# Kernel tuning notes

Measured on AMD Instinct MI355X. Metric: run time of the kernel, lower is better.

The kernel has to match this reference:

```python
import jax, jax.numpy as jnp
import numpy as np

B, P, L = 8, 196, 80
DIM1, DIM2, ATT = 2048, 300, 1024


def setup_inputs() -> dict:
    key = jax.random.key(0)
    ks = jax.random.split(key, 8)
    s1 = 1.0 / np.sqrt(DIM1)
    s2 = 1.0 / np.sqrt(DIM2)
    sa = 1.0 / np.sqrt(ATT)
    return {
        "x1": jax.random.normal(ks[0], (B, P, DIM1), jnp.float32),
        "x2": jax.random.normal(ks[1], (B, L, DIM2), jnp.float32),
        "W1": jax.random.uniform(ks[2], (ATT, DIM1), jnp.float32, -s1, s1),
        "W2": jax.random.uniform(ks[3], (ATT, DIM2), jnp.float32, -s2, s2),
        "Wh": jax.random.uniform(ks[4], (ATT, ATT), jnp.float32, -sa, sa),
        "bh": jax.random.uniform(ks[5], (ATT,), jnp.float32, -sa, sa),
        "wt": jax.random.uniform(ks[6], (ATT,), jnp.float32, -sa, sa),
        "bt": jax.random.uniform(ks[7], (), jnp.float32, -sa, sa),
    }


def reference(x1, x2, W1, W2, Wh, bh, wt, bt):
    # project: p1 (B,P,A), p2 (B,L,A)
    p1 = jnp.einsum("bpd,ad->bpa", x1, W1)
    p2 = jnp.einsum("bld,ad->bla", x2, W2)
    # broadcast bilinear + tanh: (B,L,P,A)
    h = jnp.tanh(p1[:, None, :, :] * p2[:, :, None, :])
    # hidden linear then target linear (rank-1 on last dim)
    t = jnp.einsum("blpa,ca->blpc", h, Wh) + bh
    alpha = jnp.einsum("blpc,c->blp", t, wt) + bt  # (B,L,P)
    return alpha
```

## Files before the change

kernel.cpp:

```cpp
#include <hip/hip_runtime.h>
#include <hip/hip_bf16.h>

static constexpr int kB   = 8;
static constexpr int kP   = 196;
static constexpr int kL   = 80;
static constexpr int kD1  = 2048;
static constexpr int kD2  = 300;
static constexpr int kD2p = 320;
static constexpr int kATT = 1024;
static constexpr int kM   = kB * kP;
static constexpr int kR2  = kB * kL;
static constexpr int kOut = kB * kL * kP;
static constexpr int kASplit = 16;
static constexpr int kAChunk = kATT / kASplit;
static constexpr int kLPer   = 5;

static constexpr float kTanhScale = 2.8853900817779268f;

__device__ __forceinline__ unsigned short f2bf(float x) {
    union { float f; unsigned int u; } c; c.f = x;
    unsigned int r = c.u + 0x7fffu + ((c.u >> 16) & 1u);
    return (unsigned short)(r >> 16);
}

typedef __attribute__((ext_vector_type(8))) short  bf16x8;
typedef __attribute__((ext_vector_type(4))) float  f32x4;

__device__ __forceinline__ void load_lds16(const void* g, void* l) {
    __builtin_amdgcn_global_load_lds(
        (const __attribute__((address_space(1))) void*)g,
        (__attribute__((address_space(3))) void*)l, 16, 0, 0);
}

static constexpr int kN4a = kM * kD1 / 4;
static constexpr int kN4b = kATT * kD1 / 4;
static constexpr int kN1  = kR2 * kD2p;
static constexpr int kN2  = kATT * kD2p;
static constexpr int kCastBlocks =
    (kN4a + kN4b + kN1 + kN2 + 255) / 256;

__global__ __launch_bounds__(256) void prep_kernel(
        const float* __restrict__ x1, unsigned short* __restrict__ x1b,
        const float* __restrict__ W1, unsigned short* __restrict__ W1b,
        const float* __restrict__ x2, unsigned short* __restrict__ x2b,
        const float* __restrict__ W2, unsigned short* __restrict__ W2b,
        const float* __restrict__ Wh, const float* __restrict__ wt,
        const float* __restrict__ bh, const float* __restrict__ bt,
        float* __restrict__ v, float* __restrict__ beta) {
    if (blockIdx.x >= kCastBlocks) {
        int bid = blockIdx.x - kCastBlocks;
        int ax  = bid & 3;
        int c0  = (bid >> 2) * 64;
        int a   = ax * 256 + threadIdx.x;
        float acc = 0.0f;
        #pragma unroll 8
        for (int c = c0; c < c0 + 64; ++c)
            acc = fmaf(wt[c], Wh[(size_t)c * kATT + a], acc);
        atomicAdd(&v[a], acc);
        if (ax == 0 && threadIdx.x < 64) {
            int c = c0 + threadIdx.x;
            float pb = wt[c] * bh[c];
            #pragma unroll
            for (int off = 32; off > 0; off >>= 1)
                pb += __shfl_down(pb, off, 64);
            if (threadIdx.x == 0) {
                if (c0 == 0) pb += bt[0];
                atomicAdd(beta, pb);
            }
        }
        return;
    }
    int i = blockIdx.x * 256 + threadIdx.x;
    if (i < kN4a) {
        float4 f = ((const float4*)x1)[i];
        ushort4 o = { f2bf(f.x), f2bf(f.y), f2bf(f.z), f2bf(f.w) };
        ((ushort4*)x1b)[i] = o;
    } else if ((i -= kN4a) < kN4b) {
        float4 f = ((const float4*)W1)[i];
        ushort4 o = { f2bf(f.x), f2bf(f.y), f2bf(f.z), f2bf(f.w) };
        ((ushort4*)W1b)[i] = o;
    } else if ((i -= kN4b) < kN1) {
        int r = i / kD2p, c = i - r * kD2p;
        x2b[i] = (c < kD2) ? f2bf(x2[(size_t)r * kD2 + c]) : (unsigned short)0;
    } else if ((i -= kN1) < kN2) {
        int r = i / kD2p, c = i - r * kD2p;
        W2b[i] = (c < kD2) ? f2bf(W2[(size_t)r * kD2 + c]) : (unsigned short)0;
    }
}

static constexpr int kP2Blocks = (kR2 / 64) * (kATT / 64);
static constexpr int kP1Blocks = ((kM + 63) / 64) * (kATT / 64);

__global__ __launch_bounds__(256) void gemm_all_kernel(
        const unsigned short* __restrict__ x2b, const unsigned short* __restrict__ W2b,
        float* __restrict__ p2w,
        const unsigned short* __restrict__ x1b, const unsigned short* __restrict__ W1b,
        float* __restrict__ p1w) {
    __shared__ unsigned short As[64 * 64];
    __shared__ unsigned short Bs[64 * 64];

    const unsigned short *Ab, *Bb;
    float* Co; int M, K, mx, nx; float scale;
    {
        int bid = blockIdx.x;
        if (bid < kP2Blocks) {
            Ab = x2b; Bb = W2b; Co = p2w; M = kR2; K = kD2p; scale = 1.0f;
            mx = bid % (kR2 / 64); nx = bid / (kR2 / 64);
        } else {
            int l = bid - kP2Blocks;
            Ab = x1b; Bb = W1b; Co = p1w; M = kM; K = kD1; scale = kTanhScale;
            mx = l % ((kM + 63) / 64); nx = l / ((kM + 63) / 64);
        }
    }
    const int m0   = mx * 64;
    const int n0   = nx * 64;
    const int tid  = threadIdx.x;
    const int lane = tid & 63;
    const int wv   = tid >> 6;
    const int mh   = (wv >> 1) * 32;
    const int nh   = (wv & 1) * 32;

    const int row0 = tid >> 3,         ko0 = (tid & 7) * 8;
    const int row1 = (tid + 256) >> 3, ko1 = (tid & 7) * 8;
    const int ar0 = min(m0 + row0, M - 1), ar1 = min(m0 + row1, M - 1);
    const int br0 = n0 + row0,             br1 = n0 + row1;

    f32x4 acc[2][2] = {};
    for (int k0 = 0; k0 < K; k0 += 64) {
        load_lds16(Ab + (size_t)ar0 * K + k0 + ko0, (char*)As + tid * 16);
        load_lds16(Ab + (size_t)ar1 * K + k0 + ko1, (char*)As + (tid + 256) * 16);
        load_lds16(Bb + (size_t)br0 * K + k0 + ko0, (char*)Bs + tid * 16);
        load_lds16(Bb + (size_t)br1 * K + k0 + ko1, (char*)Bs + (tid + 256) * 16);
        __syncthreads();

        #pragma unroll
        for (int kk = 0; kk < 2; ++kk) {
            bf16x8 af[2], bf[2];
            #pragma unroll
            for (int i = 0; i < 2; ++i) {
                int r = mh + i * 16 + (lane & 15);
                af[i] = *(const bf16x8*)((const char*)As + r * 128 + kk * 64 + (lane >> 4) * 16);
            }
            #pragma unroll
            for (int j = 0; j < 2; ++j) {
                int r = nh + j * 16 + (lane & 15);
                bf[j] = *(const bf16x8*)((const char*)Bs + r * 128 + kk * 64 + (lane >> 4) * 16);
            }
            #pragma unroll
            for (int i = 0; i < 2; ++i)
                #pragma unroll
                for (int j = 0; j < 2; ++j)
                    acc[i][j] = __builtin_amdgcn_mfma_f32_16x16x32_bf16(
                                    af[i], bf[j], acc[i][j], 0, 0, 0);
        }
        __syncthreads();
    }

    #pragma unroll
    for (int i = 0; i < 2; ++i)
        #pragma unroll
        for (int j = 0; j < 2; ++j)
            #pragma unroll
            for (int r = 0; r < 4; ++r) {
                int m = m0 + mh + i * 16 + (lane >> 4) * 4 + r;
                int n = n0 + nh + j * 16 + (lane & 15);
                if (m < M) Co[(size_t)m * kATT + n] = scale * acc[i][j][r];
            }
}

__global__ __launch_bounds__(256) void alpha_kernel(
        const float* __restrict__ p1, const float* __restrict__ p2,
        const float* __restrict__ v, float* __restrict__ part) {
    __shared__ float vs[kAChunk];
    __shared__ float sred;
    const int b     = blockIdx.y;
    const int as    = blockIdx.z;
    const int aBase = as * kAChunk;
    const int p0    = blockIdx.x * 16;
    const int tid   = threadIdx.x;
    const int tp    = tid & 15;
    const int lg    = tid >> 4;

    if (tid < kAChunk) vs[tid] = v[aBase + tid];
    __syncthreads();
    if (tid < 64) {
        float s = vs[tid & (kAChunk - 1)] * ((tid < kAChunk) ? 1.0f : 0.0f);
        s = vs[tid < kAChunk ? tid : 0];
        if (tid >= kAChunk) s = 0.0f;
        #pragma unroll
        for (int off = 32; off > 0; off >>= 1)
            s += __shfl_down(s, off, 64);
        if (tid == 0) sred = s;
    }
    __syncthreads();
    const float sumV = sred;

    const int p   = p0 + tp;
    const int gr1 = b * kP + min(p, kP - 1);
    const float* pu = p1 + (size_t)gr1 * kATT + aBase;
    const float* pw = p2 + ((size_t)(b * kL + lg * kLPer)) * kATT + aBase;

    float acc[kLPer] = {};
    #pragma unroll 2
    for (int a4 = 0; a4 < kAChunk / 4; ++a4) {
        float4 u  = *(const float4*)(pu + a4 * 4);
        float4 vv = *(const float4*)&vs[a4 * 4];
        #pragma unroll
        for (int j = 0; j < kLPer; ++j) {
            float4 w = *(const float4*)(pw + (size_t)j * kATT + a4 * 4);
            acc[j] = fmaf(vv.x, __builtin_amdgcn_rcpf(__builtin_amdgcn_exp2f(u.x * w.x) + 1.0f), acc[j]);
            acc[j] = fmaf(vv.y, __builtin_amdgcn_rcpf(__builtin_amdgcn_exp2f(u.y * w.y) + 1.0f), acc[j]);
            acc[j] = fmaf(vv.z, __builtin_amdgcn_rcpf(__builtin_amdgcn_exp2f(u.z * w.z) + 1.0f), acc[j]);
            acc[j] = fmaf(vv.w, __builtin_amdgcn_rcpf(__builtin_amdgcn_exp2f(u.w * w.w) + 1.0f), acc[j]);
        }
    }
    if (p < kP) {
        float* po = part + (size_t)as * kOut + ((size_t)b * kL + lg * kLPer) * kP + p;
        #pragma unroll
        for (int j = 0; j < kLPer; ++j)
            po[(size_t)j * kP] = sumV - 2.0f * acc[j];
    }
}

__global__ __launch_bounds__(256) void reduce_kernel(
        const float* __restrict__ part, const float* __restrict__ beta,
        float* __restrict__ out) {
    int i = blockIdx.x * 256 + threadIdx.x;
    if (i < kOut) {
        float s = beta[0];
        #pragma unroll
        for (int r = 0; r < kASplit; ++r)
            s += part[(size_t)r * kOut + i];
        out[i] = s;
    }
}

extern "C" void kernel_launch(void* const* d_in, const int* in_sizes, int n_in,
                              void* d_out, int out_size, void* d_ws, size_t ws_size,
                              hipStream_t stream) {
    const float* x1 = (const float*)d_in[0];
    const float* x2 = (const float*)d_in[1];
    const float* W1 = (const float*)d_in[2];
    const float* W2 = (const float*)d_in[3];
    const float* Wh = (const float*)d_in[4];
    const float* bh = (const float*)d_in[5];
    const float* wt = (const float*)d_in[6];
    const float* bt = (const float*)d_in[7];
    float* out = (float*)d_out;

    float* ws   = (float*)d_ws;
    float* v    = ws;
    float* beta = ws + 1024;
    float* p2w  = ws + 1088;
    float* p1w  = p2w + (size_t)kR2 * kATT;
    unsigned short* x1b = (unsigned short*)(p1w + (size_t)kM * kATT);
    unsigned short* W1b = x1b + (size_t)kM * kD1;
    unsigned short* x2b = W1b + (size_t)kATT * kD1;
    unsigned short* W2b = x2b + (size_t)kR2 * kD2p;
    float* part = (float*)(W2b + (size_t)kATT * kD2p);

    hipMemsetAsync(ws, 0, 1088 * sizeof(float), stream);

    prep_kernel<<<dim3(kCastBlocks + 64), 256, 0, stream>>>(
        x1, x1b, W1, W1b, x2, x2b, W2, W2b, Wh, wt, bh, bt, v, beta);
    gemm_all_kernel<<<dim3(kP2Blocks + kP1Blocks), 256, 0, stream>>>(
        x2b, W2b, p2w, x1b, W1b, p1w);
    alpha_kernel<<<dim3((kP + 15) / 16, kB, kASplit), 256, 0, stream>>>(
        p1w, p2w, v, part);
    reduce_kernel<<<dim3((kOut + 255) / 256), 256, 0, stream>>>(part, beta, out);
}
```

Baseline: 154.1 us.

## Fuse fp32-to-bf16 cast into GEMM tile staging and merge prep into GEMM

Drops the separate cast pass that wrote bf16 copies of x1, W1, x2 and W2 to global memory. Each GEMM block now loads fp32 tiles, converts them in registers, and writes bf16 into LDS. The v/beta reduction blocks move into the same launch, which saves one kernel launch and the bf16 round trip through memory. In exchange, staging uses plain register loads instead of direct global-to-LDS async loads, and A/B tiles are re-read and re-converted in fp32 by many blocks.

```diff
diff --git a/kernel.cpp b/kernel.cpp
--- a/kernel.cpp
+++ b/kernel.cpp
@@ -17,41 +17,119 @@
 
 static constexpr float kTanhScale = 2.8853900817779268f;
 
-__device__ __forceinline__ unsigned short f2bf(float x) {
-    union { float f; unsigned int u; } c; c.f = x;
-    unsigned int r = c.u + 0x7fffu + ((c.u >> 16) & 1u);
-    return (unsigned short)(r >> 16);
-}
-
 typedef __attribute__((ext_vector_type(8))) short  bf16x8;
 typedef __attribute__((ext_vector_type(4))) float  f32x4;
 
-__device__ __forceinline__ void load_lds16(const void* g, void* l) {
-    __builtin_amdgcn_global_load_lds(
-        (const __attribute__((address_space(1))) void*)g,
-        (__attribute__((address_space(3))) void*)l, 16, 0, 0);
-}
-
-static constexpr int kN4a = kM * kD1 / 4;
-static constexpr int kN4b = kATT * kD1 / 4;
-static constexpr int kN1  = kR2 * kD2p;
-static constexpr int kN2  = kATT * kD2p;
-static constexpr int kCastBlocks =
-    (kN4a + kN4b + kN1 + kN2 + 255) / 256;
-
-__global__ __launch_bounds__(256) void prep_kernel(
-        const float* __restrict__ x1, unsigned short* __restrict__ x1b,
-        const float* __restrict__ W1, unsigned short* __restrict__ W1b,
-        const float* __restrict__ x2, unsigned short* __restrict__ x2b,
-        const float* __restrict__ W2, unsigned short* __restrict__ W2b,
+__device__ __forceinline__ unsigned int pack_bf2(float lo, float hi) {
+    union { float f; unsigned int u; } a, b; a.f = lo; b.f = hi;
+    unsigned int rl = a.u + 0x7fffu + ((a.u >> 16) & 1u);
+    unsigned int rh = b.u + 0x7fffu + ((b.u >> 16) & 1u);
+    return (rl >> 16) | (rh & 0xffff0000u);
+}
+
+template<int KSRC, int KT>
+__device__ __forceinline__ void stage_tile(
+        const float* __restrict__ G, int row_g, int k0,
+        unsigned short* __restrict__ S, int tid) {
+    const int row = tid >> 2;
+    const int kq  = (tid & 3) * 16;
+    const float* src = G + (size_t)row_g * KSRC + k0 + kq;
+    unsigned int pk[8];
+    #pragma unroll
+    for (int j = 0; j < 4; ++j) {
+        float4 f = make_float4(0.f, 0.f, 0.f, 0.f);
+        if (KSRC == KT || k0 + kq + j * 4 + 4 <= KSRC)
+            f = *(const float4*)(src + j * 4);
+        pk[j * 2 + 0] = pack_bf2(f.x, f.y);
+        pk[j * 2 + 1] = pack_bf2(f.z, f.w);
+    }
+    uint4* dst = (uint4*)((char*)S + row * 128 + kq * 2);
+    dst[0] = make_uint4(pk[0], pk[1], pk[2], pk[3]);
+    dst[1] = make_uint4(pk[4], pk[5], pk[6], pk[7]);
+}
+
+template<int KSRC, int KT>
+__device__ __forceinline__ void gemm_body(
+        const float* __restrict__ Ag, const float* __restrict__ Bg,
+        float* __restrict__ Co, int M, float scale, int mx, int nx,
+        unsigned short* As, unsigned short* Bs) {
+    const int m0   = mx * 64;
+    const int n0   = nx * 64;
+    const int tid  = threadIdx.x;
+    const int lane = tid & 63;
+    const int wv   = tid >> 6;
+    const int mh   = (wv >> 1) * 32;
+    const int nh   = (wv & 1) * 32;
+    const int arow = min(m0 + (tid >> 2), M - 1);
+    const int brow = n0 + (tid >> 2);
+
+    f32x4 acc[2][2] = {};
+    for (int k0 = 0; k0 < KT; k0 += 64) {
+        __syncthreads();
+        stage_tile<KSRC, KT>(Ag, arow, k0, As, tid);
+        stage_tile<KSRC, KT>(Bg, brow, k0, Bs, tid);
+        __syncthreads();
+
+        #pragma unroll
+        for (int kk = 0; kk < 2; ++kk) {
+            bf16x8 af[2], bf[2];
+            #pragma unroll
+            for (int i = 0; i < 2; ++i) {
+                int r = mh + i * 16 + (lane & 15);
+                af[i] = *(const bf16x8*)((const char*)As + r * 128 + kk * 64 + (lane >> 4) * 16);
+            }
+            #pragma unroll
+            for (int j = 0; j < 2; ++j) {
+                int r = nh + j * 16 + (lane & 15);
+                bf[j] = *(const bf16x8*)((const char*)Bs + r * 128 + kk * 64 + (lane >> 4) * 16);
+            }
+            #pragma unroll
+            for (int i = 0; i < 2; ++i)
+                #pragma unroll
+                for (int j = 0; j < 2; ++j)
+                    acc[i][j] = __builtin_amdgcn_mfma_f32_16x16x32_bf16(
+                                    af[i], bf[j], acc[i][j], 0, 0, 0);
+        }
+    }
+
+    #pragma unroll
+    for (int i = 0; i < 2; ++i)
+        #pragma unroll
+        for (int j = 0; j < 2; ++j)
+            #pragma unroll
+            for (int r = 0; r < 4; ++r) {
+                int m = m0 + mh + i * 16 + (lane >> 4) * 4 + r;
+                int n = n0 + nh + j * 16 + (lane & 15);
+                if (m < M) Co[(size_t)m * kATT + n] = scale * acc[i][j][r];
+            }
+}
+
+static constexpr int kP2Blocks = (kR2 / 64) * (kATT / 64);
+static constexpr int kP1Blocks = ((kM + 63) / 64) * (kATT / 64);
+
+__global__ __launch_bounds__(256) void mega_kernel(
+        const float* __restrict__ x2, const float* __restrict__ W2,
+        float* __restrict__ p2w,
+        const float* __restrict__ x1, const float* __restrict__ W1,
+        float* __restrict__ p1w,
         const float* __restrict__ Wh, const float* __restrict__ wt,
         const float* __restrict__ bh, const float* __restrict__ bt,
         float* __restrict__ v, float* __restrict__ beta) {
-    if (blockIdx.x >= kCastBlocks) {
-        int bid = blockIdx.x - kCastBlocks;
-        int ax  = bid & 3;
-        int c0  = (bid >> 2) * 64;
-        int a   = ax * 256 + threadIdx.x;
+    __shared__ unsigned short As[64 * 64];
+    __shared__ unsigned short Bs[64 * 64];
+    const int bid = blockIdx.x;
+    if (bid < kP2Blocks) {
+        gemm_body<kD2, kD2p>(x2, W2, p2w, kR2, 1.0f,
+                             bid % (kR2 / 64), bid / (kR2 / 64), As, Bs);
+    } else if (bid < kP2Blocks + kP1Blocks) {
+        int l = bid - kP2Blocks;
+        gemm_body<kD1, kD1>(x1, W1, p1w, kM, kTanhScale,
+                            l % ((kM + 63) / 64), l / ((kM + 63) / 64), As, Bs);
+    } else {
+        int vb = bid - kP2Blocks - kP1Blocks;
+        int ax = vb & 3;
+        int c0 = (vb >> 2) * 64;
+        int a  = ax * 256 + threadIdx.x;
         float acc = 0.0f;
         #pragma unroll 8
         for (int c = c0; c < c0 + 64; ++c)
@@ -68,104 +146,7 @@
                 atomicAdd(beta, pb);
             }
         }
-        return;
-    }
-    int i = blockIdx.x * 256 + threadIdx.x;
-    if (i < kN4a) {
-        float4 f = ((const float4*)x1)[i];
-        ushort4 o = { f2bf(f.x), f2bf(f.y), f2bf(f.z), f2bf(f.w) };
-        ((ushort4*)x1b)[i] = o;
-    } else if ((i -= kN4a) < kN4b) {
-        float4 f = ((const float4*)W1)[i];
-        ushort4 o = { f2bf(f.x), f2bf(f.y), f2bf(f.z), f2bf(f.w) };
-        ((ushort4*)W1b)[i] = o;
-    } else if ((i -= kN4b) < kN1) {
-        int r = i / kD2p, c = i - r * kD2p;
-        x2b[i] = (c < kD2) ? f2bf(x2[(size_t)r * kD2 + c]) : (unsigned short)0;
-    } else if ((i -= kN1) < kN2) {
-        int r = i / kD2p, c = i - r * kD2p;
-        W2b[i] = (c < kD2) ? f2bf(W2[(size_t)r * kD2 + c]) : (unsigned short)0;
-    }
-}
-
-static constexpr int kP2Blocks = (kR2 / 64) * (kATT / 64);
-static constexpr int kP1Blocks = ((kM + 63) / 64) * (kATT / 64);
-
-__global__ __launch_bounds__(256) void gemm_all_kernel(
-        const unsigned short* __restrict__ x2b, const unsigned short* __restrict__ W2b,
-        float* __restrict__ p2w,
-        const unsigned short* __restrict__ x1b, const unsigned short* __restrict__ W1b,
-        float* __restrict__ p1w) {
-    __shared__ unsigned short As[64 * 64];
-    __shared__ unsigned short Bs[64 * 64];
-
-    const unsigned short *Ab, *Bb;
-    float* Co; int M, K, mx, nx; float scale;
-    {
-        int bid = blockIdx.x;
-        if (bid < kP2Blocks) {
-            Ab = x2b; Bb = W2b; Co = p2w; M = kR2; K = kD2p; scale = 1.0f;
-            mx = bid % (kR2 / 64); nx = bid / (kR2 / 64);
-        } else {
-            int l = bid - kP2Blocks;
-            Ab = x1b; Bb = W1b; Co = p1w; M = kM; K = kD1; scale = kTanhScale;
-            mx = l % ((kM + 63) / 64); nx = l / ((kM + 63) / 64);
-        }
-    }
-    const int m0   = mx * 64;
-    const int n0   = nx * 64;
-    const int tid  = threadIdx.x;
-    const int lane = tid & 63;
-    const int wv   = tid >> 6;
-    const int mh   = (wv >> 1) * 32;
-    const int nh   = (wv & 1) * 32;
-
-    const int row0 = tid >> 3,         ko0 = (tid & 7) * 8;
-    const int row1 = (tid + 256) >> 3, ko1 = (tid & 7) * 8;
-    const int ar0 = min(m0 + row0, M - 1), ar1 = min(m0 + row1, M - 1);
-    const int br0 = n0 + row0,             br1 = n0 + row1;
-
-    f32x4 acc[2][2] = {};
-    for (int k0 = 0; k0 < K; k0 += 64) {
-        load_lds16(Ab + (size_t)ar0 * K + k0 + ko0, (char*)As + tid * 16);
-        load_lds16(Ab + (size_t)ar1 * K + k0 + ko1, (char*)As + (tid + 256) * 16);
-        load_lds16(Bb + (size_t)br0 * K + k0 + ko0, (char*)Bs + tid * 16);
-        load_lds16(Bb + (size_t)br1 * K + k0 + ko1, (char*)Bs + (tid + 256) * 16);
-        __syncthreads();
-
-        #pragma unroll
-        for (int kk = 0; kk < 2; ++kk) {
-            bf16x8 af[2], bf[2];
-            #pragma unroll
-            for (int i = 0; i < 2; ++i) {
-                int r = mh + i * 16 + (lane & 15);
-                af[i] = *(const bf16x8*)((const char*)As + r * 128 + kk * 64 + (lane >> 4) * 16);
-            }
-            #pragma unroll
-            for (int j = 0; j < 2; ++j) {
-                int r = nh + j * 16 + (lane & 15);
-                bf[j] = *(const bf16x8*)((const char*)Bs + r * 128 + kk * 64 + (lane >> 4) * 16);
-            }
-            #pragma unroll
-            for (int i = 0; i < 2; ++i)
-                #pragma unroll
-                for (int j = 0; j < 2; ++j)
-                    acc[i][j] = __builtin_amdgcn_mfma_f32_16x16x32_bf16(
-                                    af[i], bf[j], acc[i][j], 0, 0, 0);
-        }
-        __syncthreads();
-    }
-
-    #pragma unroll
-    for (int i = 0; i < 2; ++i)
-        #pragma unroll
-        for (int j = 0; j < 2; ++j)
-            #pragma unroll
-            for (int r = 0; r < 4; ++r) {
-                int m = m0 + mh + i * 16 + (lane >> 4) * 4 + r;
-                int n = n0 + nh + j * 16 + (lane & 15);
-                if (m < M) Co[(size_t)m * kATT + n] = scale * acc[i][j][r];
-            }
+    }
 }
 
 __global__ __launch_bounds__(256) void alpha_kernel(
@@ -184,9 +165,7 @@
     if (tid < kAChunk) vs[tid] = v[aBase + tid];
     __syncthreads();
     if (tid < 64) {
-        float s = vs[tid & (kAChunk - 1)] * ((tid < kAChunk) ? 1.0f : 0.0f);
-        s = vs[tid < kAChunk ? tid : 0];
-        if (tid >= kAChunk) s = 0.0f;
+        float s = vs[tid];
         #pragma unroll
         for (int off = 32; off > 0; off >>= 1)
             s += __shfl_down(s, off, 64);
@@ -253,18 +232,12 @@
     float* beta = ws + 1024;
     float* p2w  = ws + 1088;
     float* p1w  = p2w + (size_t)kR2 * kATT;
-    unsigned short* x1b = (unsigned short*)(p1w + (size_t)kM * kATT);
-    unsigned short* W1b = x1b + (size_t)kM * kD1;
-    unsigned short* x2b = W1b + (size_t)kATT * kD1;
-    unsigned short* W2b = x2b + (size_t)kR2 * kD2p;
-    float* part = (float*)(W2b + (size_t)kATT * kD2p);
+    float* part = p1w + (size_t)kM * kATT;
 
     hipMemsetAsync(ws, 0, 1088 * sizeof(float), stream);
 
-    prep_kernel<<<dim3(kCastBlocks + 64), 256, 0, stream>>>(
-        x1, x1b, W1, W1b, x2, x2b, W2, W2b, Wh, wt, bh, bt, v, beta);
-    gemm_all_kernel<<<dim3(kP2Blocks + kP1Blocks), 256, 0, stream>>>(
-        x2b, W2b, p2w, x1b, W1b, p1w);
+    mega_kernel<<<dim3(kP2Blocks + kP1Blocks + 64), 256, 0, stream>>>(
+        x2, W2, p2w, x1, W1, p1w, Wh, wt, bh, bt, v, beta);
     alpha_kernel<<<dim3((kP + 15) / 16, kB, kASplit), 256, 0, stream>>>(
         p1w, p2w, v, part);
     reduce_kernel<<<dim3((kOut + 255) / 256), 256, 0, stream>>>(part, beta, out);
```

Measured after the change: 159.2 us. 1.03x slower.

## Fuse prep, GEMM, alpha and reduce into one cooperative persistent kernel

Applied to the files above, without the earlier changes.

Merges the four separate kernels into a single cooperative kernel with 1024 resident blocks. The stages are separated by grid-wide syncs, and the alpha tiles run in a grid-stride loop. The v and beta reductions are rewritten as block-local reductions without atomics, which removes the workspace memset. This is meant to cut launch overhead and the gaps between kernels. In exchange it adds grid.sync costs, concentrates the v computation in only 16 blocks, and keeps the four-kernel path as a fallback if the cooperative launch fails.

```diff
diff --git a/kernel.cpp b/kernel.cpp
--- a/kernel.cpp
+++ b/kernel.cpp
@@ -1,5 +1,8 @@
 #include <hip/hip_runtime.h>
 #include <hip/hip_bf16.h>
+#include <hip/hip_cooperative_groups.h>
+
+namespace cg = cooperative_groups;
 
 static constexpr int kB   = 8;
 static constexpr int kP   = 196;
@@ -14,8 +17,24 @@
 static constexpr int kASplit = 16;
 static constexpr int kAChunk = kATT / kASplit;
 static constexpr int kLPer   = 5;
+static constexpr int kAlphaTiles = 13 * kB * kASplit;
+static constexpr int kGrid = 1024;
 
 static constexpr float kTanhScale = 2.8853900817779268f;
+
+static constexpr int kP2Blocks = (kR2 / 64) * (kATT / 64);
+static constexpr int kP1Blocks = ((kM + 63) / 64) * (kATT / 64);
+static constexpr int kGemmBlocks = kP2Blocks + kP1Blocks;
+
+static constexpr int kD0i = kM * kD1 / 4;
+static constexpr int kD1i = kATT * kD1 / 4;
+static constexpr int kD2i = kR2 * kD2p;
+static constexpr int kD3i = kATT * kD2p;
+static constexpr int kCastTotal = kD0i + kD1i + kD2i + kD3i;
+static constexpr int kCastBlk0  = 17;
+
+typedef __attribute__((ext_vector_type(8))) short  bf16x8;
+typedef __attribute__((ext_vector_type(4))) float  f32x4;
 
 __device__ __forceinline__ unsigned short f2bf(float x) {
     union { float f; unsigned int u; } c; c.f = x;
@@ -23,116 +42,91 @@
     return (unsigned short)(r >> 16);
 }
 
-typedef __attribute__((ext_vector_type(8))) short  bf16x8;
-typedef __attribute__((ext_vector_type(4))) float  f32x4;
-
 __device__ __forceinline__ void load_lds16(const void* g, void* l) {
     __builtin_amdgcn_global_load_lds(
         (const __attribute__((address_space(1))) void*)g,
         (__attribute__((address_space(3))) void*)l, 16, 0, 0);
 }
 
-static constexpr int kN4a = kM * kD1 / 4;
-static constexpr int kN4b = kATT * kD1 / 4;
-static constexpr int kN1  = kR2 * kD2p;
-static constexpr int kN2  = kATT * kD2p;
-static constexpr int kCastBlocks =
-    (kN4a + kN4b + kN1 + kN2 + 255) / 256;
-
-__global__ __launch_bounds__(256) void prep_kernel(
+__device__ __forceinline__ void cast_items(int bid, int tid,
         const float* __restrict__ x1, unsigned short* __restrict__ x1b,
         const float* __restrict__ W1, unsigned short* __restrict__ W1b,
         const float* __restrict__ x2, unsigned short* __restrict__ x2b,
         const float* __restrict__ W2, unsigned short* __restrict__ W2b,
+        int nCastBlocks) {
+    for (int i = bid * 256 + tid; i < kCastTotal; i += nCastBlocks * 256) {
+        int j = i;
+        if (j < kD0i) {
+            float4 f = ((const float4*)x1)[j];
+            ushort4 o = { f2bf(f.x), f2bf(f.y), f2bf(f.z), f2bf(f.w) };
+            ((ushort4*)x1b)[j] = o;
+        } else if ((j -= kD0i) < kD1i) {
+            float4 f = ((const float4*)W1)[j];
+            ushort4 o = { f2bf(f.x), f2bf(f.y), f2bf(f.z), f2bf(f.w) };
+            ((ushort4*)W1b)[j] = o;
+        } else if ((j -= kD1i) < kD2i) {
+            int r = j / kD2p, c = j - r * kD2p;
+            x2b[j] = (c < kD2) ? f2bf(x2[(size_t)r * kD2 + c]) : (unsigned short)0;
+        } else {
+            j -= kD2i;
+            int r = j / kD2p, c = j - r * kD2p;
+            W2b[j] = (c < kD2) ? f2bf(W2[(size_t)r * kD2 + c]) : (unsigned short)0;
+        }
+    }
+}
+
+__device__ __forceinline__ void v_block(int bid, int tid,
         const float* __restrict__ Wh, const float* __restrict__ wt,
-        const float* __restrict__ bh, const float* __restrict__ bt,
-        float* __restrict__ v, float* __restrict__ beta) {
-    if (blockIdx.x >= kCastBlocks) {
-        int bid = blockIdx.x - kCastBlocks;
-        int ax  = bid & 3;
-        int c0  = (bid >> 2) * 64;
-        int a   = ax * 256 + threadIdx.x;
-        float acc = 0.0f;
-        #pragma unroll 8
-        for (int c = c0; c < c0 + 64; ++c)
-            acc = fmaf(wt[c], Wh[(size_t)c * kATT + a], acc);
-        atomicAdd(&v[a], acc);
-        if (ax == 0 && threadIdx.x < 64) {
-            int c = c0 + threadIdx.x;
-            float pb = wt[c] * bh[c];
-            #pragma unroll
-            for (int off = 32; off > 0; off >>= 1)
-                pb += __shfl_down(pb, off, 64);
-            if (threadIdx.x == 0) {
-                if (c0 == 0) pb += bt[0];
-                atomicAdd(beta, pb);
-            }
-        }
-        return;
-    }
-    int i = blockIdx.x * 256 + threadIdx.x;
-    if (i < kN4a) {
-        float4 f = ((const float4*)x1)[i];
-        ushort4 o = { f2bf(f.x), f2bf(f.y), f2bf(f.z), f2bf(f.w) };
-        ((ushort4*)x1b)[i] = o;
-    } else if ((i -= kN4a) < kN4b) {
-        float4 f = ((const float4*)W1)[i];
-        ushort4 o = { f2bf(f.x), f2bf(f.y), f2bf(f.z), f2bf(f.w) };
-        ((ushort4*)W1b)[i] = o;
-    } else if ((i -= kN4b) < kN1) {
-        int r = i / kD2p, c = i - r * kD2p;
-        x2b[i] = (c < kD2) ? f2bf(x2[(size_t)r * kD2 + c]) : (unsigned short)0;
-    } else if ((i -= kN1) < kN2) {
-        int r = i / kD2p, c = i - r * kD2p;
-        W2b[i] = (c < kD2) ? f2bf(W2[(size_t)r * kD2 + c]) : (unsigned short)0;
-    }
-}
-
-static constexpr int kP2Blocks = (kR2 / 64) * (kATT / 64);
-static constexpr int kP1Blocks = ((kM + 63) / 64) * (kATT / 64);
-
-__global__ __launch_bounds__(256) void gemm_all_kernel(
-        const unsigned short* __restrict__ x2b, const unsigned short* __restrict__ W2b,
-        float* __restrict__ p2w,
-        const unsigned short* __restrict__ x1b, const unsigned short* __restrict__ W1b,
-        float* __restrict__ p1w) {
-    __shared__ unsigned short As[64 * 64];
-    __shared__ unsigned short Bs[64 * 64];
-
-    const unsigned short *Ab, *Bb;
-    float* Co; int M, K, mx, nx; float scale;
-    {
-        int bid = blockIdx.x;
-        if (bid < kP2Blocks) {
-            Ab = x2b; Bb = W2b; Co = p2w; M = kR2; K = kD2p; scale = 1.0f;
-            mx = bid % (kR2 / 64); nx = bid / (kR2 / 64);
-        } else {
-            int l = bid - kP2Blocks;
-            Ab = x1b; Bb = W1b; Co = p1w; M = kM; K = kD1; scale = kTanhScale;
-            mx = l % ((kM + 63) / 64); nx = l / ((kM + 63) / 64);
-        }
-    }
+        float* __restrict__ v, float* vr ) {
+    const int a  = bid * 64 + (tid & 63);
+    const int cq = tid >> 6;
+    float acc = 0.0f;
+    #pragma unroll 8
+    for (int c = cq * 256; c < cq * 256 + 256; ++c)
+        acc = fmaf(wt[c], Wh[(size_t)c * kATT + a], acc);
+    vr[cq * 64 + (tid & 63)] = acc;
+    __syncthreads();
+    if (tid < 64)
+        v[bid * 64 + tid] = vr[tid] + vr[64 + tid] + vr[128 + tid] + vr[192 + tid];
+}
+
+__device__ __forceinline__ void beta_block(int tid,
+        const float* __restrict__ wt, const float* __restrict__ bh,
+        const float* __restrict__ bt, float* __restrict__ beta) {
+    if (tid < 64) {
+        float pb = 0.0f;
+        #pragma unroll
+        for (int j = 0; j < 16; ++j)
+            pb = fmaf(wt[tid + 64 * j], bh[tid + 64 * j], pb);
+        #pragma unroll
+        for (int off = 32; off > 0; off >>= 1)
+            pb += __shfl_down(pb, off, 64);
+        if (tid == 0) beta[0] = pb + bt[0];
+    }
+}
+
+__device__ __forceinline__ void gemm_tile(
+        const unsigned short* __restrict__ Ab, const unsigned short* __restrict__ Bb,
+        float* __restrict__ Co, int M, int K, float scale, int mx, int nx,
+        unsigned short* As, unsigned short* Bs, int tid) {
     const int m0   = mx * 64;
     const int n0   = nx * 64;
-    const int tid  = threadIdx.x;
     const int lane = tid & 63;
     const int wv   = tid >> 6;
     const int mh   = (wv >> 1) * 32;
     const int nh   = (wv & 1) * 32;
-
-    const int row0 = tid >> 3,         ko0 = (tid & 7) * 8;
-    const int row1 = (tid + 256) >> 3, ko1 = (tid & 7) * 8;
+    const int row0 = tid >> 3,         ko = (tid & 7) * 8;
+    const int row1 = (tid + 256) >> 3;
     const int ar0 = min(m0 + row0, M - 1), ar1 = min(m0 + row1, M - 1);
     const int br0 = n0 + row0,             br1 = n0 + row1;
 
     f32x4 acc[2][2] = {};
     for (int k0 = 0; k0 < K; k0 += 64) {
-        load_lds16(Ab + (size_t)ar0 * K + k0 + ko0, (char*)As + tid * 16);
-        load_lds16(Ab + (size_t)ar1 * K + k0 + ko1, (char*)As + (tid + 256) * 16);
-        load_lds16(Bb + (size_t)br0 * K + k0 + ko0, (char*)Bs + tid * 16);
-        load_lds16(Bb + (size_t)br1 * K + k0 + ko1, (char*)Bs + (tid + 256) * 16);
+        load_lds16(Ab + (size_t)ar0 * K + k0 + ko, (char*)As + tid * 16);
+        load_lds16(Ab + (size_t)ar1 * K + k0 + ko, (char*)As + (tid + 256) * 16);
+        load_lds16(Bb + (size_t)br0 * K + k0 + ko, (char*)Bs + tid * 16);
+        load_lds16(Bb + (size_t)br1 * K + k0 + ko, (char*)Bs + (tid + 256) * 16);
         __syncthreads();
-
         #pragma unroll
         for (int kk = 0; kk < 2; ++kk) {
             bf16x8 af[2], bf[2];
@@ -155,7 +149,6 @@
         }
         __syncthreads();
     }
-
     #pragma unroll
     for (int i = 0; i < 2; ++i)
         #pragma unroll
@@ -168,32 +161,43 @@
             }
 }
 
-__global__ __launch_bounds__(256) void alpha_kernel(
+__device__ __forceinline__ void gemm_dispatch(int bid, int tid,
+        const unsigned short* x1b, const unsigned short* W1b,
+        const unsigned short* x2b, const unsigned short* W2b,
+        float* p1w, float* p2w, unsigned short* As, unsigned short* Bs) {
+    if (bid < kP2Blocks) {
+        gemm_tile(x2b, W2b, p2w, kR2, kD2p, 1.0f,
+                  bid % (kR2 / 64), bid / (kR2 / 64), As, Bs, tid);
+    } else {
+        int l = bid - kP2Blocks;
+        gemm_tile(x1b, W1b, p1w, kM, kD1, kTanhScale,
+                  l % ((kM + 63) / 64), l / ((kM + 63) / 64), As, Bs, tid);
+    }
+}
+
+__device__ __forceinline__ void alpha_tile(int vb, int tid,
         const float* __restrict__ p1, const float* __restrict__ p2,
-        const float* __restrict__ v, float* __restrict__ part) {
-    __shared__ float vs[kAChunk];
-    __shared__ float sred;
-    const int b     = blockIdx.y;
-    const int as    = blockIdx.z;
+        const float* __restrict__ v, float* __restrict__ part,
+        float* vs , float* sredp ) {
+    const int px = vb % 13;
+    const int b  = (vb / 13) & (kB - 1);
+    const int as = vb / (13 * kB);
     const int aBase = as * kAChunk;
-    const int p0    = blockIdx.x * 16;
-    const int tid   = threadIdx.x;
-    const int tp    = tid & 15;
-    const int lg    = tid >> 4;
+    const int p0 = px * 16;
+    const int tp = tid & 15;
+    const int lg = tid >> 4;
 
     if (tid < kAChunk) vs[tid] = v[aBase + tid];
     __syncthreads();
     if (tid < 64) {
-        float s = vs[tid & (kAChunk - 1)] * ((tid < kAChunk) ? 1.0f : 0.0f);
-        s = vs[tid < kAChunk ? tid : 0];
-        if (tid >= kAChunk) s = 0.0f;
+        float s = vs[tid];
         #pragma unroll
         for (int off = 32; off > 0; off >>= 1)
             s += __shfl_down(s, off, 64);
-        if (tid == 0) sred = s;
+        if (tid == 0) *sredp = s;
     }
     __syncthreads();
-    const float sumV = sred;
+    const float sumV = *sredp;
 
     const int p   = p0 + tp;
     const int gr1 = b * kP + min(p, kP - 1);
@@ -222,7 +226,87 @@
     }
 }
 
-__global__ __launch_bounds__(256) void reduce_kernel(
+__global__ __launch_bounds__(256, 4) void fused_kernel(
+        const float* __restrict__ x1, const float* __restrict__ x2,
+        const float* __restrict__ W1, const float* __restrict__ W2,
+        const float* __restrict__ Wh, const float* __restrict__ bh,
+        const float* __restrict__ wt, const float* __restrict__ bt,
+        float* p2w, float* p1w, float* v, float* beta, float* part, float* out,
+        unsigned short* x1b, unsigned short* W1b,
+        unsigned short* x2b, unsigned short* W2b) {
+    __shared__ __align__(16) unsigned char smem[16384];
+    unsigned short* As = (unsigned short*)smem;
+    unsigned short* Bs = (unsigned short*)(smem + 8192);
+    float* vr    = (float*)smem;
+    float* vs    = (float*)smem;
+    float* sredp = (float*)(smem + 256);
+
+    const int bid = blockIdx.x;
+    const int tid = threadIdx.x;
+    cg::grid_group grid = cg::this_grid();
+
+    if (bid < 16)            v_block(bid, tid, Wh, wt, v, vr);
+    else if (bid == 16)      beta_block(tid, wt, bh, bt, beta);
+    else                     cast_items(bid - kCastBlk0, tid, x1, x1b, W1, W1b,
+                                        x2, x2b, W2, W2b, kGrid - kCastBlk0);
+    grid.sync();
+
+    if (bid < kGemmBlocks)
+        gemm_dispatch(bid, tid, x1b, W1b, x2b, W2b, p1w, p2w, As, Bs);
+    grid.sync();
+
+    for (int vb = bid; vb < kAlphaTiles; vb += kGrid) {
+        alpha_tile(vb, tid, p1w, p2w, v, part, vs, sredp);
+        __syncthreads();
+    }
+    grid.sync();
+
+    {
+        int i = bid * 256 + tid;
+        if (i < kOut) {
+            float s = beta[0];
+            #pragma unroll
+            for (int r = 0; r < kASplit; ++r)
+                s += part[(size_t)r * kOut + i];
+            out[i] = s;
+        }
+    }
+}
+
+__global__ __launch_bounds__(256) void prep_fb(
+        const float* __restrict__ x1, const float* __restrict__ x2,
+        const float* __restrict__ W1, const float* __restrict__ W2,
+        const float* __restrict__ Wh, const float* __restrict__ bh,
+        const float* __restrict__ wt, const float* __restrict__ bt,
+        float* v, float* beta,
+        unsigned short* x1b, unsigned short* W1b,
+        unsigned short* x2b, unsigned short* W2b) {
+    __shared__ float vr[256];
+    const int bid = blockIdx.x, tid = threadIdx.x;
+    if (bid < 16)       v_block(bid, tid, Wh, wt, v, vr);
+    else if (bid == 16) beta_block(tid, wt, bh, bt, beta);
+    else                cast_items(bid - kCastBlk0, tid, x1, x1b, W1, W1b,
+                                   x2, x2b, W2, W2b, kGrid - kCastBlk0);
+}
+
+__global__ __launch_bounds__(256) void gemm_fb(
+        const unsigned short* x1b, const unsigned short* W1b,
+        const unsigned short* x2b, const unsigned short* W2b,
+        float* p1w, float* p2w) {
+    __shared__ __align__(16) unsigned char smem[16384];
+    gemm_dispatch(blockIdx.x, threadIdx.x, x1b, W1b, x2b, W2b, p1w, p2w,
+                  (unsigned short*)smem, (unsigned short*)(smem + 8192));
+}
+
+__global__ __launch_bounds__(256) void alpha_fb(
+        const float* __restrict__ p1, const float* __restrict__ p2,
+        const float* __restrict__ v, float* __restrict__ part) {
+    __shared__ float vs[64];
+    __shared__ float sred;
+    alpha_tile(blockIdx.x, threadIdx.x, p1, p2, v, part, vs, &sred);
+}
+
+__global__ __launch_bounds__(256) void reduce_fb(
         const float* __restrict__ part, const float* __restrict__ beta,
         float* __restrict__ out) {
     int i = blockIdx.x * 256 + threadIdx.x;
@@ -253,19 +337,26 @@
     float* beta = ws + 1024;
     float* p2w  = ws + 1088;
     float* p1w  = p2w + (size_t)kR2 * kATT;
-    unsigned short* x1b = (unsigned short*)(p1w + (size_t)kM * kATT);
+    float* part = p1w + (size_t)kM * kATT;
+    unsigned short* x1b = (unsigned short*)(part + (size_t)kASplit * kOut);
     unsigned short* W1b = x1b + (size_t)kM * kD1;
     unsigned short* x2b = W1b + (size_t)kATT * kD1;
     unsigned short* W2b = x2b + (size_t)kR2 * kD2p;
-    float* part = (float*)(W2b + (size_t)kATT * kD2p);
-
-    hipMemsetAsync(ws, 0, 1088 * sizeof(float), stream);
-
-    prep_kernel<<<dim3(kCastBlocks + 64), 256, 0, stream>>>(
-        x1, x1b, W1, W1b, x2, x2b, W2, W2b, Wh, wt, bh, bt, v, beta);
-    gemm_all_kernel<<<dim3(kP2Blocks + kP1Blocks), 256, 0, stream>>>(
-        x2b, W2b, p2w, x1b, W1b, p1w);
-    alpha_kernel<<<dim3((kP + 15) / 16, kB, kASplit), 256, 0, stream>>>(
-        p1w, p2w, v, part);
-    reduce_kernel<<<dim3((kOut + 255) / 256), 256, 0, stream>>>(part, beta, out);
-}
+
+    void* args[] = { (void*)&x1, (void*)&x2, (void*)&W1, (void*)&W2,
+                     (void*)&Wh, (void*)&bh, (void*)&wt, (void*)&bt,
+                     (void*)&p2w, (void*)&p1w, (void*)&v, (void*)&beta,
+                     (void*)&part, (void*)&out,
+                     (void*)&x1b, (void*)&W1b, (void*)&x2b, (void*)&W2b };
+    hipError_t rc = hipLaunchCooperativeKernel(
+        (void*)fused_kernel, dim3(kGrid), dim3(256), args, 0, stream);
+
+    if (rc != hipSuccess) {
+        prep_fb<<<dim3(kGrid), 256, 0, stream>>>(
+            x1, x2, W1, W2, Wh, bh, wt, bt, v, beta, x1b, W1b, x2b, W2b);
+        gemm_fb<<<dim3(kGemmBlocks), 256, 0, stream>>>(
+            x1b, W1b, x2b, W2b, p1w, p2w);
+        alpha_fb<<<dim3(kAlphaTiles), 256, 0, stream>>>(p1w, p2w, v, part);
+        reduce_fb<<<dim3((kOut + 255) / 256), 256, 0, stream>>>(part, beta, out);
+    }
+}
```

After: 526.4 us. 242% more time.

## Swizzle GEMM LDS layout and drop atomics and memset in prep

Applied to the files above, without the earlier changes.

The GEMM stores each 16-byte chunk of a row at an XOR-swizzled slot in LDS so that MFMA fragment reads hit fewer bank conflicts. The prep kernel now computes v = Wh^T·wt with one block per 64 columns, reducing in shared memory, and beta in a dedicated block. This removes the atomics and the hipMemsetAsync launch. The workspace layout is also reordered so the partial buffer comes before the bf16 copies.

```diff
diff --git a/kernel.cpp b/kernel.cpp
--- a/kernel.cpp
+++ b/kernel.cpp
@@ -17,27 +17,28 @@
 
 static constexpr float kTanhScale = 2.8853900817779268f;
 
+typedef __attribute__((ext_vector_type(8))) short  bf16x8;
+typedef __attribute__((ext_vector_type(4))) float  f32x4;
+
 __device__ __forceinline__ unsigned short f2bf(float x) {
     union { float f; unsigned int u; } c; c.f = x;
     unsigned int r = c.u + 0x7fffu + ((c.u >> 16) & 1u);
     return (unsigned short)(r >> 16);
 }
 
-typedef __attribute__((ext_vector_type(8))) short  bf16x8;
-typedef __attribute__((ext_vector_type(4))) float  f32x4;
-
 __device__ __forceinline__ void load_lds16(const void* g, void* l) {
     __builtin_amdgcn_global_load_lds(
         (const __attribute__((address_space(1))) void*)g,
         (__attribute__((address_space(3))) void*)l, 16, 0, 0);
 }
 
-static constexpr int kN4a = kM * kD1 / 4;
-static constexpr int kN4b = kATT * kD1 / 4;
-static constexpr int kN1  = kR2 * kD2p;
-static constexpr int kN2  = kATT * kD2p;
-static constexpr int kCastBlocks =
-    (kN4a + kN4b + kN1 + kN2 + 255) / 256;
+static constexpr int kD0i = kM * kD1 / 4;
+static constexpr int kD1i = kATT * kD1 / 4;
+static constexpr int kD2i = kR2 * kD2p;
+static constexpr int kD3i = kATT * kD2p;
+static constexpr int kCastTotal  = kD0i + kD1i + kD2i + kD3i;
+static constexpr int kCastBlocks = (kCastTotal + 255) / 256;
+static constexpr int kPrepBlocks = 17 + kCastBlocks;
 
 __global__ __launch_bounds__(256) void prep_kernel(
         const float* __restrict__ x1, unsigned short* __restrict__ x1b,
@@ -47,42 +48,47 @@
         const float* __restrict__ Wh, const float* __restrict__ wt,
         const float* __restrict__ bh, const float* __restrict__ bt,
         float* __restrict__ v, float* __restrict__ beta) {
-    if (blockIdx.x >= kCastBlocks) {
-        int bid = blockIdx.x - kCastBlocks;
-        int ax  = bid & 3;
-        int c0  = (bid >> 2) * 64;
-        int a   = ax * 256 + threadIdx.x;
+    __shared__ float vr[256];
+    const int bid = blockIdx.x, tid = threadIdx.x;
+    if (bid < 16) {
+        const int a  = bid * 64 + (tid & 63);
+        const int cq = tid >> 6;
         float acc = 0.0f;
         #pragma unroll 8
-        for (int c = c0; c < c0 + 64; ++c)
+        for (int c = cq * 256; c < cq * 256 + 256; ++c)
             acc = fmaf(wt[c], Wh[(size_t)c * kATT + a], acc);
-        atomicAdd(&v[a], acc);
-        if (ax == 0 && threadIdx.x < 64) {
-            int c = c0 + threadIdx.x;
-            float pb = wt[c] * bh[c];
+        vr[cq * 64 + (tid & 63)] = acc;
+        __syncthreads();
+        if (tid < 64)
+            v[bid * 64 + tid] = vr[tid] + vr[64 + tid] + vr[128 + tid] + vr[192 + tid];
+        return;
+    }
+    if (bid == 16) {
+        if (tid < 64) {
+            float pb = 0.0f;
+            #pragma unroll
+            for (int j = 0; j < 16; ++j)
+                pb = fmaf(wt[tid + 64 * j], bh[tid + 64 * j], pb);
             #pragma unroll
             for (int off = 32; off > 0; off >>= 1)
                 pb += __shfl_down(pb, off, 64);
-            if (threadIdx.x == 0) {
-                if (c0 == 0) pb += bt[0];
-                atomicAdd(beta, pb);
-            }
+            if (tid == 0) beta[0] = pb + bt[0];
         }
         return;
     }
-    int i = blockIdx.x * 256 + threadIdx.x;
-    if (i < kN4a) {
+    int i = (bid - 17) * 256 + tid;
+    if (i < kD0i) {
         float4 f = ((const float4*)x1)[i];
         ushort4 o = { f2bf(f.x), f2bf(f.y), f2bf(f.z), f2bf(f.w) };
         ((ushort4*)x1b)[i] = o;
-    } else if ((i -= kN4a) < kN4b) {
+    } else if ((i -= kD0i) < kD1i) {
         float4 f = ((const float4*)W1)[i];
         ushort4 o = { f2bf(f.x), f2bf(f.y), f2bf(f.z), f2bf(f.w) };
         ((ushort4*)W1b)[i] = o;
-    } else if ((i -= kN4b) < kN1) {
+    } else if ((i -= kD1i) < kD2i) {
         int r = i / kD2p, c = i - r * kD2p;
         x2b[i] = (c < kD2) ? f2bf(x2[(size_t)r * kD2 + c]) : (unsigned short)0;
-    } else if ((i -= kN1) < kN2) {
+    } else if ((i -= kD2i) < kD3i) {
         int r = i / kD2p, c = i - r * kD2p;
         W2b[i] = (c < kD2) ? f2bf(W2[(size_t)r * kD2 + c]) : (unsigned short)0;
     }
@@ -120,31 +126,32 @@
     const int mh   = (wv >> 1) * 32;
     const int nh   = (wv & 1) * 32;
 
-    const int row0 = tid >> 3,         ko0 = (tid & 7) * 8;
-    const int row1 = (tid + 256) >> 3, ko1 = (tid & 7) * 8;
-    const int ar0 = min(m0 + row0, M - 1), ar1 = min(m0 + row1, M - 1);
-    const int br0 = n0 + row0,             br1 = n0 + row1;
+    const int srow = tid >> 3;
+    const int ko   = (((tid & 7) ^ (srow & 7))) * 8;
+    const int ar0 = min(m0 + srow, M - 1), ar1 = min(m0 + srow + 32, M - 1);
+    const int br0 = n0 + srow,             br1 = n0 + srow + 32;
 
     f32x4 acc[2][2] = {};
     for (int k0 = 0; k0 < K; k0 += 64) {
-        load_lds16(Ab + (size_t)ar0 * K + k0 + ko0, (char*)As + tid * 16);
-        load_lds16(Ab + (size_t)ar1 * K + k0 + ko1, (char*)As + (tid + 256) * 16);
-        load_lds16(Bb + (size_t)br0 * K + k0 + ko0, (char*)Bs + tid * 16);
-        load_lds16(Bb + (size_t)br1 * K + k0 + ko1, (char*)Bs + (tid + 256) * 16);
+        load_lds16(Ab + (size_t)ar0 * K + k0 + ko, (char*)As + tid * 16);
+        load_lds16(Ab + (size_t)ar1 * K + k0 + ko, (char*)As + (tid + 256) * 16);
+        load_lds16(Bb + (size_t)br0 * K + k0 + ko, (char*)Bs + tid * 16);
+        load_lds16(Bb + (size_t)br1 * K + k0 + ko, (char*)Bs + (tid + 256) * 16);
         __syncthreads();
-
         #pragma unroll
         for (int kk = 0; kk < 2; ++kk) {
             bf16x8 af[2], bf[2];
             #pragma unroll
             for (int i = 0; i < 2; ++i) {
                 int r = mh + i * 16 + (lane & 15);
-                af[i] = *(const bf16x8*)((const char*)As + r * 128 + kk * 64 + (lane >> 4) * 16);
+                int s = (kk * 4 + (lane >> 4)) ^ (r & 7);
+                af[i] = *(const bf16x8*)((const char*)As + r * 128 + s * 16);
             }
             #pragma unroll
             for (int j = 0; j < 2; ++j) {
                 int r = nh + j * 16 + (lane & 15);
-                bf[j] = *(const bf16x8*)((const char*)Bs + r * 128 + kk * 64 + (lane >> 4) * 16);
+                int s = (kk * 4 + (lane >> 4)) ^ (r & 7);
+                bf[j] = *(const bf16x8*)((const char*)Bs + r * 128 + s * 16);
             }
             #pragma unroll
             for (int i = 0; i < 2; ++i)
@@ -184,9 +191,7 @@
     if (tid < kAChunk) vs[tid] = v[aBase + tid];
     __syncthreads();
     if (tid < 64) {
-        float s = vs[tid & (kAChunk - 1)] * ((tid < kAChunk) ? 1.0f : 0.0f);
-        s = vs[tid < kAChunk ? tid : 0];
-        if (tid >= kAChunk) s = 0.0f;
+        float s = vs[tid];
         #pragma unroll
         for (int off = 32; off > 0; off >>= 1)
             s += __shfl_down(s, off, 64);
@@ -253,15 +258,13 @@
     float* beta = ws + 1024;
     float* p2w  = ws + 1088;
     float* p1w  = p2w + (size_t)kR2 * kATT;
-    unsigned short* x1b = (unsigned short*)(p1w + (size_t)kM * kATT);
+    float* part = p1w + (size_t)kM * kATT;
+    unsigned short* x1b = (unsigned short*)(part + (size_t)kASplit * kOut);
     unsigned short* W1b = x1b + (size_t)kM * kD1;
     unsigned short* x2b = W1b + (size_t)kATT * kD1;
     unsigned short* W2b = x2b + (size_t)kR2 * kD2p;
-    float* part = (float*)(W2b + (size_t)kATT * kD2p);
-
-    hipMemsetAsync(ws, 0, 1088 * sizeof(float), stream);
-
-    prep_kernel<<<dim3(kCastBlocks + 64), 256, 0, stream>>>(
+
+    prep_kernel<<<dim3(kPrepBlocks), 256, 0, stream>>>(
         x1, x1b, W1, W1b, x2, x2b, W2, W2b, Wh, wt, bh, bt, v, beta);
     gemm_all_kernel<<<dim3(kP2Blocks + kP1Blocks), 256, 0, stream>>>(
         x2b, W2b, p2w, x1b, W1b, p1w);
```

Result: slower. 161.7 us (+4.9%).
